# Performance work log

Measured on AMD Instinct MI355X. Metric: run time of the kernel, lower is better.

## Reference

```python
import jax, jax.numpy as jnp
import numpy as np

B, L, D, M_MAX = 4, 4096, 1024, 512


def setup_inputs() -> dict:
    key = jax.random.key(0)
    k_ct, k_enc, k_lo, k_hi, k_w = jax.random.split(key, 5)
    concept_tokens = jax.random.normal(k_ct, (B, M_MAX, D), dtype=jnp.float32)
    encoder_out = jax.random.normal(k_enc, (B, L, D), dtype=jnp.float32)
    # sorted unique boundary positions per batch, first boundary at position 0
    rng = np.random.RandomState(0)
    idx = np.stack([np.sort(rng.choice(np.arange(1, L), size=M_MAX - 1, replace=False)) for _ in range(B)])
    boundary_idx = jnp.asarray(np.concatenate([np.zeros((B, 1), dtype=np.int64), idx], axis=1))  # [B, M_max]
    # probs < 0.5 everywhere except at boundary positions (>= 0.5), so cumsum(mask)-1 < M_max
    lo = jax.random.uniform(k_lo, (B, L), minval=0.02, maxval=0.48)
    hi = jax.random.uniform(k_hi, (B, M_MAX), minval=0.5, maxval=1.0)
    rows = jnp.arange(B)[:, None]
    boundary_probs = lo.at[rows, boundary_idx].set(hi)
    concept_mask = jnp.ones((B, M_MAX), dtype=bool)
    W = jax.random.normal(k_w, (D, D), dtype=jnp.float32) * 0.02  # residual_proj.weight (out = x @ W.T)
    return {"concept_tokens": concept_tokens, "encoder_out": encoder_out,
            "boundary_probs": boundary_probs, "boundary_idx": boundary_idx,
            "concept_mask": concept_mask, "W": W}


def _ema_smooth(concept_tokens, p_at_bounds):
    """h_i = (1-p_i)*h_{i-1} + p_i*c_i via associative scan; h_0 = c_0."""
    h0 = concept_tokens[:, 0]                                  # [B, d]
    p_rest = p_at_bounds[:, 1:]                                # [B, M-1]
    decay = jnp.clip(1.0 - p_rest, 1e-7, None)
    b = p_rest[..., None] * concept_tokens[:, 1:]              # [B, M-1, d]
    a = jnp.broadcast_to(decay[..., None], b.shape)

    def combine(x, y):
        a1, b1 = x
        a2, b2 = y
        return a1 * a2, a2 * b1 + b2

    A, Bc = jax.lax.associative_scan(combine, (a, b), axis=1)
    h_rest = A * h0[:, None, :] + Bc                           # h_i = A_i*h0 + B_i
    return jnp.concatenate([h0[:, None, :], h_rest], axis=1)   # [B, M, d]


def reference(concept_tokens, encoder_out, boundary_probs, boundary_idx, concept_mask, W):
    d = encoder_out.shape[-1]
    # Eq.5: EMA over concept tokens with boundary probs gathered at boundary positions
    p_raw = jnp.take_along_axis(boundary_probs, boundary_idx, axis=1)          # [B, M]
    p_at_bounds = jnp.where(concept_mask, p_raw, 1.0)
    p_at_bounds = jnp.clip(p_at_bounds, 0.1, None)
    smoothed = _ema_smooth(concept_tokens, p_at_bounds)                        # [B, M, d]
    # Eq.8: plug-back via running boundary count
    boundary_mask = boundary_probs >= 0.5                                      # [B, L]
    plug_back_idx = jnp.clip(jnp.cumsum(boundary_mask.astype(jnp.int32), axis=1) - 1, 0, None)
    plugback = jnp.take_along_axis(smoothed, plug_back_idx[..., None], axis=1)  # [B, L, d]
    # Eq.6/7/9: confidence + STE (forward value is exactly 1.0)
    b_f = boundary_mask.astype(boundary_probs.dtype)
    c_t = b_f * boundary_probs + (1.0 - b_f) * (1.0 - boundary_probs)
    ste_c = c_t + jax.lax.stop_gradient(1.0 - c_t)
    upsampled = ste_c[..., None] * plugback
    # Eq.3: residual linear (no bias)
    return upsampled + jnp.einsum('bld,ed->ble', encoder_out, W)
```

## Files before the change

### kernel.cpp

```cpp
#include <hip/hip_runtime.h>
#include <hip/hip_bf16.h>
#include <stdint.h>


#define B_  4
#define L_  4096
#define D_  1024
#define M_  512

typedef __attribute__((ext_vector_type(8))) short bf16x8;
typedef __attribute__((ext_vector_type(4))) float f32x4;
typedef __attribute__((ext_vector_type(8))) unsigned short u16x8;

__device__ inline unsigned short f2bf(float f) {
    unsigned u = __float_as_uint(f);
    u += 0x7fffu + ((u >> 16) & 1u);
    return (unsigned short)(u >> 16);
}

__global__ void prep_all_kernel(const float* __restrict__ enc, const float* __restrict__ W,
                                const float* __restrict__ probs, const float* __restrict__ ct,
                                const int* __restrict__ bidx,
                                unsigned short* __restrict__ encb, unsigned short* __restrict__ Wb,
                                int* __restrict__ pbi, float* __restrict__ smoothed,
                                int encBlocks) {
    __shared__ int part[512];
    __shared__ float ad[M_], bdp[M_];
    __shared__ float Ac[8][64], Bc[8][64], Hin[8][64];

    const int blk = blockIdx.x;
    const int t   = threadIdx.x;

    if (blk < encBlocks + 256) {
        const float* src; unsigned short* dst; size_t i;
        if (blk < encBlocks) { src = enc; dst = encb; i = (size_t)blk * 512 + t; }
        else                 { src = W;   dst = Wb;   i = (size_t)(blk - encBlocks) * 512 + t; }
        float4 x0 = ((const float4*)src)[2 * i];
        float4 x1 = ((const float4*)src)[2 * i + 1];
        u16x8 v;
        v[0] = f2bf(x0.x); v[1] = f2bf(x0.y); v[2] = f2bf(x0.z); v[3] = f2bf(x0.w);
        v[4] = f2bf(x1.x); v[5] = f2bf(x1.y); v[6] = f2bf(x1.z); v[7] = f2bf(x1.w);
        ((u16x8*)dst)[i] = v;
    } else if (blk < encBlocks + 260) {
        int b = blk - (encBlocks + 256);
        const float4* pr = (const float4*)(probs + b * L_);
        int cnt[8]; int s = 0;
        #pragma unroll
        for (int u = 0; u < 2; ++u) {
            float4 x = pr[t * 2 + u];
            s += (x.x >= 0.5f); cnt[u * 4 + 0] = s;
            s += (x.y >= 0.5f); cnt[u * 4 + 1] = s;
            s += (x.z >= 0.5f); cnt[u * 4 + 2] = s;
            s += (x.w >= 0.5f); cnt[u * 4 + 3] = s;
        }
        part[t] = s;
        __syncthreads();
        for (int off = 1; off < 512; off <<= 1) {
            int x = part[t];
            int y = (t >= off) ? part[t - off] : 0;
            __syncthreads();
            part[t] = x + y;
            __syncthreads();
        }
        int excl = part[t] - s;
        int4* po = (int4*)(pbi + b * L_ + t * 8);
        #pragma unroll
        for (int u = 0; u < 2; ++u) {
            int4 o;
            o.x = max(excl + cnt[u * 4 + 0] - 1, 0);
            o.y = max(excl + cnt[u * 4 + 1] - 1, 0);
            o.z = max(excl + cnt[u * 4 + 2] - 1, 0);
            o.w = max(excl + cnt[u * 4 + 3] - 1, 0);
            po[u] = o;
        }
    } else {
        int idx = blk - (encBlocks + 260);
        int b  = idx >> 4;
        int d0 = (idx & 15) * 64;
        int dl = t & 63;
        int ch = t >> 6;
        {
            int m = t;
            int bi = bidx[b * M_ + m];
            float p = fmaxf(probs[b * L_ + bi], 0.1f);
            ad[m]  = (m == 0) ? 0.0f : fmaxf(1.0f - p, 1e-7f);
            bdp[m] = (m == 0) ? 1.0f : p;
        }
        __syncthreads();
        const float* ctp = ct + ((size_t)b * M_ + ch * 64) * D_ + d0 + dl;
        float A = 1.0f, Bv = 0.0f;
        #pragma unroll 8
        for (int i = 0; i < 64; ++i) {
            int m = ch * 64 + i;
            float c = ctp[(size_t)i * D_];
            A  = ad[m] * A;
            Bv = ad[m] * Bv + bdp[m] * c;
        }
        Ac[ch][dl] = A; Bc[ch][dl] = Bv;
        __syncthreads();
        if (t < 64) {
            float H = 0.0f;
            #pragma unroll
            for (int c = 0; c < 8; ++c) {
                Hin[c][t] = H;
                H = Ac[c][t] * H + Bc[c][t];
            }
        }
        __syncthreads();
        float h = Hin[ch][dl];
        float* smp = smoothed + ((size_t)b * M_ + ch * 64) * D_ + d0 + dl;
        #pragma unroll 8
        for (int i = 0; i < 64; ++i) {
            int m = ch * 64 + i;
            float c = ctp[(size_t)i * D_];
            h = ad[m] * h + bdp[m] * c;
            smp[(size_t)i * D_] = h;
        }
    }
}

#define NT_ 32

__global__ __launch_bounds__(512, 1) void gemm3_kernel(
    const unsigned short* __restrict__ encb, const unsigned short* __restrict__ Wb,
    const float* __restrict__ smoothed, const int* __restrict__ pbi,
    float* __restrict__ out)
{
    __shared__ __align__(16) unsigned short As[3][256 * 32];
    __shared__ __align__(16) unsigned short Bs[3][256 * 32];

    const int tid  = threadIdx.x;
    const int lane = tid & 63;
    const int w    = tid >> 6;
    const int wm   = w >> 2;
    const int wn   = w & 3;
    const int l15  = lane & 15;
    const int l16  = lane >> 4;

    const int orig = blockIdx.x;
    const int rm   = (orig & 7) * 32 + (orig >> 3);
    const size_t rowBase = (size_t)(rm >> 2) * 256;
    const int    colBase = (rm & 3) * 256;

    const int rsw = (((lane & 3) ^ ((lane >> 2) & 3)) << 3);

#define STAGE(kt, s)                                                                     \
  {                                                                                      \
    _Pragma("unroll")                                                                    \
    for (int i_ = 0; i_ < 2; ++i_) {                                                     \
      int row_ = i_ * 128 + w * 16 + (lane >> 2);                                        \
      const unsigned short* ga_ = encb + (rowBase + row_) * D_ + (kt) * 32 + rsw;        \
      __builtin_amdgcn_global_load_lds(                                                  \
          (const __attribute__((address_space(1))) void*)ga_,                            \
          (__attribute__((address_space(3))) void*)&As[s][i_ * 4096 + w * 512], 16, 0, 0);\
      const unsigned short* gb_ = Wb + (size_t)(colBase + row_) * D_ + (kt) * 32 + rsw;  \
      __builtin_amdgcn_global_load_lds(                                                  \
          (const __attribute__((address_space(1))) void*)gb_,                            \
          (__attribute__((address_space(3))) void*)&Bs[s][i_ * 4096 + w * 512], 16, 0, 0);\
    }                                                                                    \
  }

    f32x4 acc[8][4] = {};

    STAGE(0, 0);
    STAGE(1, 1);
    asm volatile("s_waitcnt vmcnt(4)" ::: "memory");
    __builtin_amdgcn_s_barrier();
    __builtin_amdgcn_sched_barrier(0);

    int s = 0;
    for (int t = 0; t < NT_; ++t) {
        const char* aB = (const char*)As[s];
        const char* bB = (const char*)Bs[s];
        const int swz = (l15 & 3) << 4;
        bf16x8 a[8], bb[4];
        #pragma unroll
        for (int m = 0; m < 8; ++m)
            a[m] = *(const bf16x8*)(aB + (wm * 128 + m * 16 + l15) * 64 + ((l16 * 16) ^ swz));
        #pragma unroll
        for (int n = 0; n < 4; ++n)
            bb[n] = *(const bf16x8*)(bB + (wn * 64 + n * 16 + l15) * 64 + ((l16 * 16) ^ swz));

        int s2 = s + 2; if (s2 >= 3) s2 -= 3;
        if (t + 2 < NT_) STAGE(t + 2, s2);

        __builtin_amdgcn_s_setprio(1);
        #pragma unroll
        for (int m = 0; m < 8; ++m)
            #pragma unroll
            for (int n = 0; n < 4; ++n)
                acc[m][n] = __builtin_amdgcn_mfma_f32_16x16x32_bf16(a[m], bb[n], acc[m][n], 0, 0, 0);
        __builtin_amdgcn_s_setprio(0);

        if (t + 1 < NT_) {
            if (t + 2 < NT_) { asm volatile("s_waitcnt vmcnt(4)" ::: "memory"); }
            else             { asm volatile("s_waitcnt vmcnt(0)" ::: "memory"); }
            __builtin_amdgcn_s_barrier();
            __builtin_amdgcn_sched_barrier(0);
        }
        s += 1; if (s >= 3) s -= 3;
    }
#undef STAGE

    #pragma unroll
    for (int m = 0; m < 8; ++m) {
        const size_t row0 = rowBase + wm * 128 + m * 16;
        #pragma unroll
        for (int j = 0; j < 4; ++j) {
            size_t row = row0 + l16 * 4 + j;
            int b  = (int)(row >> 12);
            int pb = pbi[row];
            pb = pb < (M_ - 1) ? pb : (M_ - 1);
            const float* sm = smoothed + ((size_t)(b * M_ + pb)) * D_;
            #pragma unroll
            for (int n = 0; n < 4; ++n) {
                int col = colBase + wn * 64 + n * 16 + l15;
                out[row * D_ + col] = acc[m][n][j] + sm[col];
            }
        }
    }
}

#define LDP 72
__global__ __launch_bounds__(256, 2) void gemm_fused_kernel(
    const float* __restrict__ enc, const unsigned short* __restrict__ Wb,
    const float* __restrict__ smoothed, const int* __restrict__ pbi,
    float* __restrict__ out)
{
    __shared__ unsigned short Asf[128][LDP];
    __shared__ unsigned short Bsf[128][LDP];
    const int tid  = threadIdx.x;
    const int lane = tid & 63;
    const int wid  = tid >> 6;
    const int wm   = wid >> 1;
    const int wn   = wid & 1;
    const int l15  = lane & 15;
    const int l16  = lane >> 4;
    const size_t rowBase = (size_t)blockIdx.x * 128;
    const int    colBase = blockIdx.y * 128;
    f32x4 acc[4][4] = {};
    for (int t = 0; t < D_ / 64; ++t) {
        const int k0 = t * 64;
        #pragma unroll
        for (int i = 0; i < 4; ++i) {
            int c = i * 256 + tid;
            int r = c >> 3;
            int c8 = c & 7;
            const float4* g = (const float4*)(enc + (rowBase + r) * D_ + k0 + c8 * 8);
            float4 x0 = g[0];
            float4 x1 = g[1];
            u16x8 v;
            v[0] = f2bf(x0.x); v[1] = f2bf(x0.y); v[2] = f2bf(x0.z); v[3] = f2bf(x0.w);
            v[4] = f2bf(x1.x); v[5] = f2bf(x1.y); v[6] = f2bf(x1.z); v[7] = f2bf(x1.w);
            *(u16x8*)&Asf[r][c8 * 8] = v;
        }
        #pragma unroll
        for (int i = 0; i < 4; ++i) {
            int c = i * 256 + tid;
            int r = c >> 3;
            int c8 = c & 7;
            u16x8 v = *(const u16x8*)(Wb + (size_t)(colBase + r) * D_ + k0 + c8 * 8);
            *(u16x8*)&Bsf[r][c8 * 8] = v;
        }
        __syncthreads();
        #pragma unroll
        for (int kk = 0; kk < 2; ++kk) {
            bf16x8 a[4], bbf[4];
            #pragma unroll
            for (int m = 0; m < 4; ++m)
                a[m] = *(const bf16x8*)&Asf[wm * 64 + m * 16 + l15][kk * 32 + l16 * 8];
            #pragma unroll
            for (int n = 0; n < 4; ++n)
                bbf[n] = *(const bf16x8*)&Bsf[wn * 64 + n * 16 + l15][kk * 32 + l16 * 8];
            #pragma unroll
            for (int m = 0; m < 4; ++m)
                #pragma unroll
                for (int n = 0; n < 4; ++n)
                    acc[m][n] = __builtin_amdgcn_mfma_f32_16x16x32_bf16(a[m], bbf[n], acc[m][n], 0, 0, 0);
        }
        __syncthreads();
    }
    #pragma unroll
    for (int m = 0; m < 4; ++m) {
        #pragma unroll
        for (int j = 0; j < 4; ++j) {
            size_t row = rowBase + wm * 64 + m * 16 + l16 * 4 + j;
            int b  = (int)(row >> 12);
            int pb = pbi[row];
            pb = pb < (M_ - 1) ? pb : (M_ - 1);
            const float* sm = smoothed + ((size_t)(b * M_ + pb)) * D_;
            #pragma unroll
            for (int n = 0; n < 4; ++n) {
                int col = colBase + wn * 64 + n * 16 + l15;
                out[row * D_ + col] = acc[m][n][j] + sm[col];
            }
        }
    }
}

extern "C" void kernel_launch(void* const* d_in, const int* in_sizes, int n_in,
                              void* d_out, int out_size, void* d_ws, size_t ws_size,
                              hipStream_t stream) {
    const float* ct    = (const float*)d_in[0];
    const float* enc   = (const float*)d_in[1];
    const float* probs = (const float*)d_in[2];
    const int*   bidx  = (const int*)d_in[3];
    const float* W     = (const float*)d_in[5];
    float* out = (float*)d_out;
    char*  ws  = (char*)d_ws;

    const size_t SZ_ENCB = (size_t)B_ * L_ * D_ * 2;
    const size_t SZ_SM   = (size_t)B_ * M_ * D_ * 4;
    const size_t SZ_PBI  = (size_t)B_ * L_ * 4;
    const size_t SZ_WB   = (size_t)D_ * D_ * 2;

    if (ws_size >= SZ_ENCB + SZ_SM + SZ_PBI + SZ_WB) {
        unsigned short* encb     = (unsigned short*)ws;
        float*          smoothed = (float*)(ws + SZ_ENCB);
        int*            pbi      = (int*)(ws + SZ_ENCB + SZ_SM);
        unsigned short* Wb       = (unsigned short*)(ws + SZ_ENCB + SZ_SM + SZ_PBI);

        const int encBlocks = B_ * L_ * D_ / 4096;
        const int nBlocks   = encBlocks + 256 + B_ + B_ * D_ / 64;
        hipLaunchKernelGGL(prep_all_kernel, dim3(nBlocks), dim3(512), 0, stream,
                           enc, W, probs, ct, bidx, encb, Wb, pbi, smoothed, encBlocks);
        hipLaunchKernelGGL(gemm3_kernel, dim3(256), dim3(512), 0, stream,
                           encb, Wb, smoothed, pbi, out);
    } else {
        float*          smoothed = (float*)ws;
        int*            pbi      = (int*)(ws + SZ_SM);
        unsigned short* Wb       = (unsigned short*)(ws + SZ_SM + SZ_PBI);
        const int nBlocks = 0 + 256 + B_ + B_ * D_ / 64;
        hipLaunchKernelGGL(prep_all_kernel, dim3(nBlocks), dim3(512), 0, stream,
                           enc, W, probs, ct, bidx, (unsigned short*)ws , Wb, pbi, smoothed, 0);
        hipLaunchKernelGGL(gemm_fused_kernel, dim3(B_ * L_ / 128, D_ / 128), dim3(256), 0, stream,
                           enc, Wb, smoothed, pbi, out);
    }
}
```

Baseline: 171.1 us.

## Restructure bf16 GEMM into 8-phase ping-pong schedule with K=64 tiles

```diff
diff --git a/kernel.cpp b/kernel.cpp
--- a/kernel.cpp
+++ b/kernel.cpp
@@ -119,15 +119,14 @@
     }
 }
 
-#define NT_ 32
-
-__global__ __launch_bounds__(512, 1) void gemm3_kernel(
+#define NTT 16
+
+__global__ __launch_bounds__(512, 2) void gemm8_kernel(
     const unsigned short* __restrict__ encb, const unsigned short* __restrict__ Wb,
     const float* __restrict__ smoothed, const int* __restrict__ pbi,
     float* __restrict__ out)
 {
-    __shared__ __align__(16) unsigned short As[3][256 * 32];
-    __shared__ __align__(16) unsigned short Bs[3][256 * 32];
+    __shared__ __align__(16) char smem[131072];
 
     const int tid  = threadIdx.x;
     const int lane = tid & 63;
@@ -142,65 +141,109 @@
     const size_t rowBase = (size_t)(rm >> 2) * 256;
     const int    colBase = (rm & 3) * 256;
 
-    const int rsw = (((lane & 3) ^ ((lane >> 2) & 3)) << 3);
-
-#define STAGE(kt, s)                                                                     \
-  {                                                                                      \
-    _Pragma("unroll")                                                                    \
-    for (int i_ = 0; i_ < 2; ++i_) {                                                     \
-      int row_ = i_ * 128 + w * 16 + (lane >> 2);                                        \
-      const unsigned short* ga_ = encb + (rowBase + row_) * D_ + (kt) * 32 + rsw;        \
-      __builtin_amdgcn_global_load_lds(                                                  \
-          (const __attribute__((address_space(1))) void*)ga_,                            \
-          (__attribute__((address_space(3))) void*)&As[s][i_ * 4096 + w * 512], 16, 0, 0);\
-      const unsigned short* gb_ = Wb + (size_t)(colBase + row_) * D_ + (kt) * 32 + rsw;  \
-      __builtin_amdgcn_global_load_lds(                                                  \
-          (const __attribute__((address_space(1))) void*)gb_,                            \
-          (__attribute__((address_space(3))) void*)&Bs[s][i_ * 4096 + w * 512], 16, 0, 0);\
-    }                                                                                    \
-  }
+    const int rsw5  = ((l15 >> 2) & 1) << 5;
+    const int colb0 = (0 + l16 * 16) ^ rsw5;
+    const int colb1 = (64 + l16 * 16) ^ rsw5;
+
+    const int aRd0 = (0 + wm) * 16384 + l15 * 128;
+    const int aRd1 = (2 + wm) * 16384 + l15 * 128;
+    const int bRd0 = 65536 + (0 + (wn >> 1)) * 16384 + ((wn & 1) * 64 + l15) * 128;
+    const int bRd1 = 65536 + (2 + (wn >> 1)) * 16384 + ((wn & 1) * 64 + l15) * 128;
+
+    const int srow  = tid >> 3;
+    const int sslot = (tid & 7) ^ (((tid >> 5) & 1) << 1);
+    const unsigned short* aSrc = encb + (rowBase + srow) * D_ + sslot * 8;
+    const unsigned short* bSrc = Wb + ((size_t)colBase + srow) * D_ + sslot * 8;
+
+#define STAGE_A(T, db, h)                                                                 \
+  { _Pragma("unroll") for (int i_ = 0; i_ < 2; ++i_) {                                    \
+      const unsigned short* g_ = aSrc + (size_t)((h) * 128 + i_ * 64) * D_ + (T) * 64;    \
+      __builtin_amdgcn_global_load_lds(                                                   \
+          (const __attribute__((address_space(1))) void*)g_,                              \
+          (__attribute__((address_space(3))) void*)(smem + ((db)*2+(h))*16384 + i_*8192 + tid*16), \
+          16, 0, 0); } }
+
+#define STAGE_B(T, db, h)                                                                 \
+  { _Pragma("unroll") for (int i_ = 0; i_ < 2; ++i_) {                                    \
+      const unsigned short* g_ = bSrc + (size_t)((h) * 128 + i_ * 64) * D_ + (T) * 64;    \
+      __builtin_amdgcn_global_load_lds(                                                   \
+          (const __attribute__((address_space(1))) void*)g_,                              \
+          (__attribute__((address_space(3))) void*)(smem + 65536 + ((db)*2+(h))*16384 + i_*8192 + tid*16), \
+          16, 0, 0); } }
+
+#define LDSA(aRd, mbase)                                                                  \
+  { _Pragma("unroll") for (int m_ = 0; m_ < 4; ++m_) {                                    \
+      a[m_*2+0] = *(const bf16x8*)(smem + (aRd) + ((mbase)+m_)*2048 + colb0);             \
+      a[m_*2+1] = *(const bf16x8*)(smem + (aRd) + ((mbase)+m_)*2048 + colb1); } }
+
+#define LDSB(bRd, nbase)                                                                  \
+  { _Pragma("unroll") for (int n_ = 0; n_ < 2; ++n_) {                                    \
+      b[((nbase)+n_)*2+0] = *(const bf16x8*)(smem + (bRd) + ((nbase)+n_)*2048 + colb0);   \
+      b[((nbase)+n_)*2+1] = *(const bf16x8*)(smem + (bRd) + ((nbase)+n_)*2048 + colb1); } }
+
+#define MFMA_Q(mbase, nbase)                                                              \
+  { _Pragma("unroll") for (int m_ = 0; m_ < 4; ++m_)                                      \
+    _Pragma("unroll") for (int n_ = 0; n_ < 2; ++n_) {                                    \
+      acc[(mbase)+m_][(nbase)+n_] = __builtin_amdgcn_mfma_f32_16x16x32_bf16(              \
+          a[m_*2+0], b[((nbase)+n_)*2+0], acc[(mbase)+m_][(nbase)+n_], 0, 0, 0);          \
+      acc[(mbase)+m_][(nbase)+n_] = __builtin_amdgcn_mfma_f32_16x16x32_bf16(              \
+          a[m_*2+1], b[((nbase)+n_)*2+1], acc[(mbase)+m_][(nbase)+n_], 0, 0, 0); } }
+
+#define PH_OPEN()  do { __builtin_amdgcn_sched_barrier(0); __builtin_amdgcn_s_barrier();  \
+    __builtin_amdgcn_sched_barrier(0);                                                    \
+    asm volatile("s_waitcnt lgkmcnt(0)" ::: "memory");                                    \
+    __builtin_amdgcn_sched_barrier(0); __builtin_amdgcn_s_setprio(1); } while (0)
+
+#define PH_CLOSE() do { __builtin_amdgcn_s_setprio(0); __builtin_amdgcn_sched_barrier(0); \
+    __builtin_amdgcn_s_barrier(); __builtin_amdgcn_sched_barrier(0); } while (0)
 
     f32x4 acc[8][4] = {};
-
-    STAGE(0, 0);
-    STAGE(1, 1);
+    bf16x8 a[8], b[8];
+
+    STAGE_A(0, 0, 0); STAGE_A(0, 0, 1);
+    STAGE_B(0, 0, 0); STAGE_B(0, 0, 1);
+    STAGE_B(1, 1, 0); STAGE_B(1, 1, 1);
     asm volatile("s_waitcnt vmcnt(4)" ::: "memory");
     __builtin_amdgcn_s_barrier();
     __builtin_amdgcn_sched_barrier(0);
 
-    int s = 0;
-    for (int t = 0; t < NT_; ++t) {
-        const char* aB = (const char*)As[s];
-        const char* bB = (const char*)Bs[s];
-        const int swz = (l15 & 3) << 4;
-        bf16x8 a[8], bb[4];
-        #pragma unroll
-        for (int m = 0; m < 8; ++m)
-            a[m] = *(const bf16x8*)(aB + (wm * 128 + m * 16 + l15) * 64 + ((l16 * 16) ^ swz));
-        #pragma unroll
-        for (int n = 0; n < 4; ++n)
-            bb[n] = *(const bf16x8*)(bB + (wn * 64 + n * 16 + l15) * 64 + ((l16 * 16) ^ swz));
-
-        int s2 = s + 2; if (s2 >= 3) s2 -= 3;
-        if (t + 2 < NT_) STAGE(t + 2, s2);
-
-        __builtin_amdgcn_s_setprio(1);
-        #pragma unroll
-        for (int m = 0; m < 8; ++m)
-            #pragma unroll
-            for (int n = 0; n < 4; ++n)
-                acc[m][n] = __builtin_amdgcn_mfma_f32_16x16x32_bf16(a[m], bb[n], acc[m][n], 0, 0, 0);
-        __builtin_amdgcn_s_setprio(0);
-
-        if (t + 1 < NT_) {
-            if (t + 2 < NT_) { asm volatile("s_waitcnt vmcnt(4)" ::: "memory"); }
-            else             { asm volatile("s_waitcnt vmcnt(0)" ::: "memory"); }
-            __builtin_amdgcn_s_barrier();
-            __builtin_amdgcn_sched_barrier(0);
-        }
-        s += 1; if (s >= 3) s -= 3;
-    }
-#undef STAGE
+    #pragma unroll 1
+    for (int i = 0; i < NTT / 2; ++i) {
+        const int t1 = 2 * i + 1;
+        const int t2 = (2 * i + 2 < NTT) ? 2 * i + 2 : NTT - 1;
+        const int t3 = (2 * i + 3 < NTT) ? 2 * i + 3 : NTT - 1;
+        LDSA(aRd0, 0); LDSB(bRd0, 0);
+        STAGE_A(t1, 1, 0);
+        PH_OPEN(); MFMA_Q(0, 0); PH_CLOSE();
+        LDSB(bRd0, 2);
+        STAGE_A(t1, 1, 1);
+        PH_OPEN(); MFMA_Q(0, 2); PH_CLOSE();
+        LDSA(aRd0, 4);
+        STAGE_B(t2, 0, 0);
+        PH_OPEN(); MFMA_Q(4, 0); PH_CLOSE();
+        STAGE_B(t2, 0, 1);
+        asm volatile("s_waitcnt vmcnt(4)" ::: "memory");
+        PH_OPEN(); MFMA_Q(4, 2); PH_CLOSE();
+        LDSA(aRd1, 0); LDSB(bRd1, 0);
+        STAGE_A(t2, 0, 0);
+        PH_OPEN(); MFMA_Q(0, 0); PH_CLOSE();
+        LDSB(bRd1, 2);
+        STAGE_A(t2, 0, 1);
+        PH_OPEN(); MFMA_Q(0, 2); PH_CLOSE();
+        LDSA(aRd1, 4);
+        STAGE_B(t3, 1, 0);
+        PH_OPEN(); MFMA_Q(4, 0); PH_CLOSE();
+        STAGE_B(t3, 1, 1);
+        asm volatile("s_waitcnt vmcnt(4)" ::: "memory");
+        PH_OPEN(); MFMA_Q(4, 2); PH_CLOSE();
+    }
+#undef STAGE_A
+#undef STAGE_B
+#undef LDSA
+#undef LDSB
+#undef MFMA_Q
+#undef PH_OPEN
+#undef PH_CLOSE
 
     #pragma unroll
     for (int m = 0; m < 8; ++m) {
@@ -208,10 +251,10 @@
         #pragma unroll
         for (int j = 0; j < 4; ++j) {
             size_t row = row0 + l16 * 4 + j;
-            int b  = (int)(row >> 12);
-            int pb = pbi[row];
+            int bb2 = (int)(row >> 12);
+            int pb  = pbi[row];
             pb = pb < (M_ - 1) ? pb : (M_ - 1);
-            const float* sm = smoothed + ((size_t)(b * M_ + pb)) * D_;
+            const float* sm = smoothed + ((size_t)(bb2 * M_ + pb)) * D_;
             #pragma unroll
             for (int n = 0; n < 4; ++n) {
                 int col = colBase + wn * 64 + n * 16 + l15;
@@ -324,7 +367,7 @@
         const int nBlocks   = encBlocks + 256 + B_ + B_ * D_ / 64;
         hipLaunchKernelGGL(prep_all_kernel, dim3(nBlocks), dim3(512), 0, stream,
                            enc, W, probs, ct, bidx, encb, Wb, pbi, smoothed, encBlocks);
-        hipLaunchKernelGGL(gemm3_kernel, dim3(256), dim3(512), 0, stream,
+        hipLaunchKernelGGL(gemm8_kernel, dim3(256), dim3(512), 0, stream,
                            encb, Wb, smoothed, pbi, out);
     } else {
         float*          smoothed = (float*)ws;
```

Result: no change. 173.2 us (+1.3%).
